# Optimization experiments

Hardware: AMD Instinct MI355X
Metric: run time of the kernel (lower is better)

Reference implementation:

```python
import jax, jax.numpy as jnp
import numpy as np

ATT_WIDTH = 512  # attention_width from init

def _band_mask(T, width, dtype):
    # tf.matrix_band_part(ones, width//2, (width-1)//2): keep i-j<=lower and j-i<=upper
    lower = width // 2
    upper = (width - 1) // 2
    i = jnp.arange(T)[:, None]
    j = jnp.arange(T)[None, :]
    keep = (i - j <= lower) & (j - i <= upper)
    return keep.astype(dtype)

def setup_inputs() -> dict:
    key = jax.random.key(0)
    k1, k2, k3, k4 = jax.random.split(key, 4)
    B, T, H, D = 8, 2048, 1024, 1024
    scale = 1.0 / np.sqrt(H)  # keep activations sane
    return {
        "inputs": jax.random.normal(k1, (B, T, H), dtype=jnp.float32),
        "WQ": jax.random.normal(k2, (H, D), dtype=jnp.float32) * scale,
        "WK": jax.random.normal(k3, (H, D), dtype=jnp.float32) * scale,
        "WV": jax.random.normal(k4, (H, D), dtype=jnp.float32) * scale,
    }

def reference(inputs, WQ, WK, WV) -> jnp.ndarray:
    B, T, H = inputs.shape
    D = WQ.shape[1]
    scale = jnp.asarray(D, inputs.dtype) ** 0.5
    q = jnp.einsum('bth,hd->btd', inputs, WQ)
    k = jnp.einsum('bth,hd->btd', inputs, WK)
    v = jnp.einsum('bth,hd->btd', inputs, WV)
    score = jnp.einsum('bqd,bkd->bqk', q, k) / scale  # [B,T,T]
    # NOTE: original multiplies score by the 0/1 band mask BEFORE softmax
    # (masked entries become 0, not -inf). Faithful reproduction.
    local = _band_mask(T, ATT_WIDTH, score.dtype)
    score = score * local[None, :, :]
    attn = jax.nn.softmax(score, axis=-1)
    return jnp.einsum('bqk,bkd->bqd', attn, v)
```

## Files before the change

### kernel.cpp

```cpp
#include <hip/hip_runtime.h>
#include <hip/hip_bf16.h>
#include <stdint.h>

typedef __attribute__((ext_vector_type(8))) short bf16x8;
typedef __attribute__((ext_vector_type(4))) short short4v;
typedef __attribute__((ext_vector_type(4))) float f32x4;

#define DEV static __device__ __forceinline__

DEV float bf2f(short u) {
    union { float f; uint32_t i; } c; c.i = ((uint32_t)(uint16_t)u) << 16; return c.f;
}
DEV short f2bf(float f) {
    union { float f; uint32_t i; } c; c.f = f;
    uint32_t i = c.i;
    uint32_t r = i + 0x7FFFu + ((i >> 16) & 1u);
    return (short)(r >> 16);
}

DEV void gload_lds16(const short* g, short* l) {
    __builtin_amdgcn_global_load_lds(
        (const __attribute__((address_space(1))) void*)g,
        (__attribute__((address_space(3))) void*)l,
        16, 0, 0);
}

__global__ __launch_bounds__(256)
void cvt_f32_bf16(const float* __restrict__ in, short* __restrict__ out) {
    long i = ((long)blockIdx.x * 256 + threadIdx.x) * 8;
    float4 a = *(const float4*)&in[i];
    float4 b = *(const float4*)&in[i + 4];
    bf16x8 o;
    o[0] = f2bf(a.x); o[1] = f2bf(a.y); o[2] = f2bf(a.z); o[3] = f2bf(a.w);
    o[4] = f2bf(b.x); o[5] = f2bf(b.y); o[6] = f2bf(b.z); o[7] = f2bf(b.w);
    *(bf16x8*)&out[i] = o;
}

__global__ __launch_bounds__(256)
void cvt2_f32_bf16(const float* __restrict__ inA, short* __restrict__ outA,
                   const float* __restrict__ inB, short* __restrict__ outB) {
    int blk = blockIdx.x;
    const float* in = (blk < 512) ? inA : inB;
    short* out      = (blk < 512) ? outA : outB;
    long i = ((long)(blk & 511) * 256 + threadIdx.x) * 8;
    float4 a = *(const float4*)&in[i];
    float4 b = *(const float4*)&in[i + 4];
    bf16x8 o;
    o[0] = f2bf(a.x); o[1] = f2bf(a.y); o[2] = f2bf(a.z); o[3] = f2bf(a.w);
    o[4] = f2bf(b.x); o[5] = f2bf(b.y); o[6] = f2bf(b.z); o[7] = f2bf(b.w);
    *(bf16x8*)&out[i] = o;
}

__global__ __launch_bounds__(256)
void transpose_w(const float* __restrict__ W, short* __restrict__ Wt) {
    const int HD = 1024;
    __shared__ float tile[32][33];
    int bx = blockIdx.x, by = blockIdx.y;
    int tx = threadIdx.x & 31, ty = threadIdx.x >> 5;
    #pragma unroll
    for (int r = ty; r < 32; r += 8)
        tile[r][tx] = W[(long)(by * 32 + r) * HD + bx * 32 + tx];
    __syncthreads();
    #pragma unroll
    for (int r = ty; r < 32; r += 8)
        Wt[(long)(bx * 32 + r) * HD + by * 32 + tx] = f2bf(tile[tx][r]);
}

__global__ __launch_bounds__(256)
void reduce_mt(const float* __restrict__ Mpart, short* __restrict__ MTb) {
    const long SL = 1024L * 1024;
    long i = ((long)blockIdx.x * 256 + threadIdx.x) * 8;
    float s[8];
    #pragma unroll
    for (int j = 0; j < 8; ++j) s[j] = 0.f;
    #pragma unroll
    for (int sl = 0; sl < 4; ++sl) {
        float4 a = *(const float4*)&Mpart[sl * SL + i];
        float4 b = *(const float4*)&Mpart[sl * SL + i + 4];
        s[0] += a.x; s[1] += a.y; s[2] += a.z; s[3] += a.w;
        s[4] += b.x; s[5] += b.y; s[6] += b.z; s[7] += b.w;
    }
    bf16x8 o;
    #pragma unroll
    for (int j = 0; j < 8; ++j) o[j] = f2bf(s[j]);
    *(bf16x8*)&MTb[i] = o;
}


DEV void stage_half(const short* __restrict__ src, int ld, short* dst, int tid) {
    int rr = tid >> 3;
    int cs = ((tid & 7) ^ (rr & 7)) << 3;
    short* d = dst + ((tid >> 6) << 9);
    gload_lds16(src + (long)rr * ld + cs, d);
    gload_lds16(src + (long)(rr + 64) * ld + cs, d + 4096);
}

DEV bf16x8 ld_frag(const short* half, int rowbase, int ks, int lane) {
    int row = rowbase + (lane & 15);
    int idx = (row << 6) + ks * 32 + ((lane >> 4) << 3);
    idx ^= (lane & 7) << 3;
    return *(const bf16x8*)&half[idx];
}

#define SCHED0 __builtin_amdgcn_sched_barrier(0)
#define SBAR do { SCHED0; __builtin_amdgcn_s_barrier(); SCHED0; } while (0)
#define VM(n)  do { asm volatile("s_waitcnt vmcnt(" #n ")" ::: "memory"); SCHED0; } while (0)
#define PRIO1 __builtin_amdgcn_s_setprio(1)
#define PRIO0 __builtin_amdgcn_s_setprio(0)

#define READ_A(HP, QM)                                                          \
    do { _Pragma("unroll") for (int iq = 0; iq < 4; ++iq)                       \
         _Pragma("unroll") for (int ks = 0; ks < 2; ++ks)                       \
             ra[iq][ks] = ld_frag(HP, (QM)*64 + iq*16, ks, lane); } while (0)

#define READ_B(HP, QN)                                                          \
    do { _Pragma("unroll") for (int jn = 0; jn < 2; ++jn)                       \
         _Pragma("unroll") for (int ks = 0; ks < 2; ++ks)                       \
             rb[QN][jn][ks] = ld_frag(HP, wn1*64 + (QN)*32 + jn*16, ks, lane); } while (0)

#define MFMA_Q(QM, QN)                                                          \
    do { _Pragma("unroll") for (int iq = 0; iq < 4; ++iq)                       \
         _Pragma("unroll") for (int jn = 0; jn < 2; ++jn)                       \
         _Pragma("unroll") for (int ks = 0; ks < 2; ++ks)                       \
             acc[(QM)*4+iq][(QN)*2+jn] = __builtin_amdgcn_mfma_f32_16x16x32_bf16( \
                 ra[iq][ks], rb[QN][jn][ks], acc[(QM)*4+iq][(QN)*2+jn], 0,0,0); } while (0)

template<int EPI>
__global__ __launch_bounds__(512, 2)
void gemm256(const short* __restrict__ Abase, const short* __restrict__ Bbase,
             void* __restrict__ o0, void* __restrict__ o1, void* __restrict__ o2,
             const float* __restrict__ Crow, const float* __restrict__ Vsum)
{
    const int T = 2048, HD = 1024;
    __shared__ __align__(16) short lds[2][2][2][8192];

    const int tid  = threadIdx.x;
    const int lane = tid & 63;
    const int w    = tid >> 6;
    const int wm   = w >> 2;
    const int wn   = w & 3;
    const int wn1  = wn & 1;

    int m0, n0, klo, khi, ldA, ldB, bz;
    const short *A, *B;
    if (EPI == 0) {
        int p = (int)blockIdx.x + 8 * (int)blockIdx.y;
        int lid = (p & 7) * 64 + (p >> 3);
        m0 = (lid >> 3) * 256; n0 = (lid & 7) * 256;
        klo = 0; khi = 1024; ldA = HD; ldB = HD; bz = 0;
        A = Abase; B = Bbase;
    } else if (EPI == 1) {
        int p = (int)blockIdx.x + 3 * ((int)blockIdx.y + 8 * (int)blockIdx.z);
        bz = p & 7; int rem = p >> 3;
        int mb = rem / 3, kb = mb + rem % 3 - 1;
        if (kb < 0 || kb > 7) return;
        m0 = mb * 256; n0 = kb * 256;
        klo = 0; khi = 1024; ldA = HD; ldB = HD;
        A = Abase + (long)bz * T * HD; B = Bbase + (long)bz * T * HD;
    } else if (EPI == 2) {
        int p = (int)blockIdx.x + 4 * ((int)blockIdx.y + 8 * (int)blockIdx.z);
        bz = p & 7; int rem = p >> 3;
        int mb = rem / 4;
        m0 = mb * 256; n0 = (rem % 4) * 256;
        klo = max(m0 - 256, 0); khi = min(m0 + 512, T);
        ldA = T; ldB = T;
        A = Abase + (long)bz * T * T; B = Bbase + (long)bz * HD * T;
    } else {
        m0 = blockIdx.y * 256; n0 = blockIdx.x * 256;
        klo = (int)blockIdx.z * 256; khi = klo + 256;
        ldA = HD; ldB = HD; bz = 0;
        A = Abase; B = Bbase;
    }

    const short* Asrc = A + (long)m0 * ldA + klo;
    const short* Bsrc = B + (long)n0 * ldB + klo;
    const short* hA0 = &lds[0][0][wm][0];
    const short* hA1 = &lds[1][0][wm][0];
    const short* hB0 = &lds[0][1][wn >> 1][0];
    const short* hB1 = &lds[1][1][wn >> 1][0];

    auto stA = [&](int bf, int hf, int t) {
        stage_half(Asrc + (long)hf * 128 * ldA + t * 64, ldA, (short*)&lds[bf][0][hf][0], tid); };
    auto stB = [&](int bf, int hf, int t) {
        stage_half(Bsrc + (long)hf * 128 * ldB + t * 64, ldB, (short*)&lds[bf][1][hf][0], tid); };

    f32x4 acc[8][4];
    #pragma unroll
    for (int i = 0; i < 8; ++i)
        #pragma unroll
        for (int j = 0; j < 4; ++j) { acc[i][j][0]=0.f; acc[i][j][1]=0.f; acc[i][j][2]=0.f; acc[i][j][3]=0.f; }
    bf16x8 ra[4][2];
    bf16x8 rb[2][2][2];

    const int NT = (khi - klo) >> 6;

    stB(0,0,0); stB(0,1,0); stA(0,0,0); stA(0,1,0); stB(1,0,1); stB(1,1,1);
    SCHED0; VM(4); SBAR;
    READ_B(hB0, 0); SCHED0;

    #pragma unroll 1
    for (int i = 0; i < NT/2 - 1; ++i) {
        int t1 = 2*i+1, t2 = 2*i+2, t3 = 2*i+3;
        SBAR; READ_A(hA0,0); SCHED0; READ_B(hB0,1); SCHED0; stA(1,0,t1); SCHED0;
        PRIO1; MFMA_Q(0,0); PRIO0; SCHED0;
        SBAR; stA(1,1,t1); SCHED0; PRIO1; MFMA_Q(0,1); PRIO0; SCHED0;
        SBAR; READ_A(hA0,1); SCHED0; stB(0,0,t2); SCHED0;
        PRIO1; MFMA_Q(1,0); PRIO0; SCHED0; VM(2); SCHED0;
        SBAR; READ_B(hB1,0); SCHED0; stB(0,1,t2); SCHED0;
        PRIO1; MFMA_Q(1,1); PRIO0; SCHED0;
        SBAR; READ_A(hA1,0); SCHED0; READ_B(hB1,1); SCHED0; stA(0,0,t2); SCHED0;
        PRIO1; MFMA_Q(0,0); PRIO0; SCHED0;
        SBAR; stA(0,1,t2); SCHED0; PRIO1; MFMA_Q(0,1); PRIO0; SCHED0;
        SBAR; READ_A(hA1,1); SCHED0; stB(1,0,t3); SCHED0;
        PRIO1; MFMA_Q(1,0); PRIO0; SCHED0; VM(2); SCHED0;
        SBAR; READ_B(hB0,0); SCHED0; stB(1,1,t3); SCHED0;
        PRIO1; MFMA_Q(1,1); PRIO0; SCHED0;
    }
    {
        int t1 = NT - 1;
        SBAR; READ_A(hA0,0); SCHED0; READ_B(hB0,1); SCHED0; stA(1,0,t1); SCHED0;
        PRIO1; MFMA_Q(0,0); PRIO0; SCHED0;
        SBAR; stA(1,1,t1); SCHED0; PRIO1; MFMA_Q(0,1); PRIO0; SCHED0;
        SBAR; READ_A(hA0,1); SCHED0;
        PRIO1; MFMA_Q(1,0); PRIO0; SCHED0; VM(0); SCHED0;
        SBAR; READ_B(hB1,0); SCHED0; PRIO1; MFMA_Q(1,1); PRIO0; SCHED0;
        SBAR; READ_A(hA1,0); SCHED0; READ_B(hB1,1); SCHED0;
        PRIO1; MFMA_Q(0,0); PRIO0; SCHED0;
        SBAR; PRIO1; MFMA_Q(0,1); PRIO0; SCHED0;
        SBAR; READ_A(hA1,1); SCHED0; PRIO1; MFMA_Q(1,0); PRIO0; SCHED0;
        SBAR; PRIO1; MFMA_Q(1,1); PRIO0; SCHED0;
    }

    const int fr = lane & 15, fq = lane >> 4;
    const int rbase = m0 + wm * 128, cbase = n0 + wn * 64;

    if (EPI == 0) {
        const int wsel = n0 >> 10;
        if (wsel == 0) {
            short* dst = (short*)o0;
            #pragma unroll
            for (int mi = 0; mi < 8; ++mi)
                #pragma unroll
                for (int ni = 0; ni < 4; ++ni)
                    #pragma unroll
                    for (int r = 0; r < 4; ++r) {
                        int row = rbase + mi * 16 + fq * 4 + r;
                        int col = cbase + ni * 16 + fr;
                        dst[(long)row * HD + col] = f2bf(acc[mi][ni][r]);
                    }
        } else {
            short* Vt = (short*)o2;
            #pragma unroll
            for (int mi = 0; mi < 8; ++mi)
                #pragma unroll
                for (int ni = 0; ni < 4; ++ni) {
                    int col  = (cbase + ni * 16 + fr) & 1023;
                    int row0 = rbase + mi * 16 + fq * 4;
                    int b = row0 >> 11, t = row0 & 2047;
                    short4v v;
                    #pragma unroll
                    for (int r = 0; r < 4; ++r) v[r] = f2bf(acc[mi][ni][r]);
                    *(short4v*)&Vt[((long)b * HD + col) * T + t] = v;
                }
        }
    } else if (EPI == 1) {
        short* S = (short*)o0 + (long)bz * T * T;
        #pragma unroll
        for (int mi = 0; mi < 8; ++mi)
            #pragma unroll
            for (int ni = 0; ni < 4; ++ni)
                #pragma unroll
                for (int r = 0; r < 4; ++r) {
                    int i = rbase + mi * 16 + fq * 4 + r;
                    int j = cbase + ni * 16 + fr;
                    bool keep = (i - j <= 256) && (j - i <= 255);
                    S[(long)i * T + j] = f2bf(keep ? acc[mi][ni][r] * (1.f/32.f) : 0.f);
                }
    } else if (EPI == 2) {
        float* out = (float*)o0;
        #pragma unroll
        for (int mi = 0; mi < 8; ++mi)
            #pragma unroll
            for (int r = 0; r < 4; ++r) {
                int i = rbase + mi * 16 + fq * 4 + r;
                float ci = Crow[bz * T + i];
                #pragma unroll
                for (int ni = 0; ni < 4; ++ni) {
                    int col = cbase + ni * 16 + fr;
                    out[((long)bz * T + i) * HD + col] = acc[mi][ni][r] + ci * Vsum[bz * HD + col];
                }
            }
    } else {
        float* dst = (float*)o0 + (long)blockIdx.z * HD * HD;
        #pragma unroll
        for (int mi = 0; mi < 8; ++mi)
            #pragma unroll
            for (int ni = 0; ni < 4; ++ni)
                #pragma unroll
                for (int r = 0; r < 4; ++r) {
                    int row = rbase + mi * 16 + fq * 4 + r;
                    int col = cbase + ni * 16 + fr;
                    dst[(long)row * HD + col] = acc[mi][ni][r];
                }
    }
}

__global__ __launch_bounds__(256)
void softmax_band(short* __restrict__ S, float* __restrict__ Crow) {
    const int T = 2048;
    int wid = (int)blockIdx.x * 4 + (threadIdx.x >> 6);
    int lane = threadIdx.x & 63;
    int b = wid >> 11, t = wid & 2047;
    int mb = t >> 7;
    int tlo = max(mb - 2, 0) * 128;
    int thi = min(mb + 2, 15) * 128 + 128;
    int nvec = (thi - tlo) >> 3;
    short* row = S + ((long)b * T + t) * T + tlo;

    bool h0 = lane < nvec;
    bool h1 = lane + 64 < nvec;
    bf16x8 v0, v1;
    float f0[8], f1[8];
    float m = 0.f;
    if (h0) {
        v0 = *(const bf16x8*)&row[lane * 8];
        #pragma unroll
        for (int j = 0; j < 8; ++j) { f0[j] = bf2f(v0[j]); m = fmaxf(m, f0[j]); }
    }
    if (h1) {
        v1 = *(const bf16x8*)&row[(lane + 64) * 8];
        #pragma unroll
        for (int j = 0; j < 8; ++j) { f1[j] = bf2f(v1[j]); m = fmaxf(m, f1[j]); }
    }
    #pragma unroll
    for (int o = 32; o; o >>= 1) m = fmaxf(m, __shfl_xor(m, o));

    float e0[8], e1[8];
    float sum = 0.f;
    if (h0) {
        #pragma unroll
        for (int j = 0; j < 8; ++j) { e0[j] = __expf(f0[j] - m); sum += e0[j]; }
    }
    if (h1) {
        #pragma unroll
        for (int j = 0; j < 8; ++j) { e1[j] = __expf(f1[j] - m); sum += e1[j]; }
    }
    #pragma unroll
    for (int o = 32; o; o >>= 1) sum += __shfl_xor(sum, o);
    float em = __expf(-m);
    sum += (float)(2048 - nvec * 8) * em;
    float inv = 1.f / sum;
    float c = em * inv;

    if (h0) {
        #pragma unroll
        for (int j = 0; j < 8; ++j) v0[j] = f2bf(e0[j] * inv - c);
        *(bf16x8*)&row[lane * 8] = v0;
    }
    if (h1) {
        #pragma unroll
        for (int j = 0; j < 8; ++j) v1[j] = f2bf(e1[j] * inv - c);
        *(bf16x8*)&row[(lane + 64) * 8] = v1;
    }
    if (lane == 0) Crow[wid] = c;
}

__global__ __launch_bounds__(256)
void vsum_rows(const short* __restrict__ Vt, float* __restrict__ Vsum) {
    int rowid = (int)blockIdx.x * 4 + (threadIdx.x >> 6);
    int lane = threadIdx.x & 63;
    const short* r = Vt + (long)rowid * 2048;
    float s = 0.f;
    #pragma unroll
    for (int v = 0; v < 4; ++v) {
        bf16x8 x = *(const bf16x8*)&r[(lane + v * 64) * 8];
        #pragma unroll
        for (int j = 0; j < 8; ++j) s += bf2f(x[j]);
    }
    #pragma unroll
    for (int o = 32; o; o >>= 1) s += __shfl_xor(s, o);
    if (lane == 0) Vsum[rowid] = s;
}

extern "C" void kernel_launch(void* const* d_in, const int* in_sizes, int n_in,
                              void* d_out, int out_size, void* d_ws, size_t ws_size,
                              hipStream_t stream) {
    const int B = 8, T = 2048, H = 1024, D = 1024;
    const long MT = (long)B * T;

    const float* X  = (const float*)d_in[0];
    const float* WQ = (const float*)d_in[1];
    const float* WK = (const float*)d_in[2];
    const float* WV = (const float*)d_in[3];
    float* out = (float*)d_out;

    char* ws = (char*)d_ws;
    size_t off = 0;
    auto alloc = [&](size_t bytes) {
        char* p = ws + off;
        off += (bytes + 255) & ~(size_t)255;
        return p;
    };
    short* Xb    = (short*)alloc(MT * H * 2);
    short* WQb   = (short*)alloc((long)H * D * 2);
    short* WKb   = (short*)alloc((long)H * D * 2);
    short* Bfuse = (short*)alloc(2L * D * H * 2);
    short* MTb   = Bfuse;
    short* WVt   = Bfuse + (long)D * H;
    float* Mpart = (float*)alloc(4L * D * H * 4);
    short* Gb    = (short*)alloc(MT * D * 2);
    short* Vt    = (short*)alloc((long)B * D * T * 2);
    short* S     = (short*)alloc((long)B * T * T * 2);
    float* Crow  = (float*)alloc(MT * 4);
    float* Vsum  = (float*)alloc((long)B * D * 4);
    if (off > ws_size) return;

    cvt_f32_bf16<<<(int)(MT * H / 2048), 256, 0, stream>>>(X, Xb);
    cvt2_f32_bf16<<<1024, 256, 0, stream>>>(WQ, WQb, WK, WKb);
    transpose_w<<<dim3(32, 32), 256, 0, stream>>>(WV, WVt);

    gemm256<3><<<dim3(4, 4, 4), 512, 0, stream>>>(WKb, WQb, Mpart, nullptr, nullptr, nullptr, nullptr);
    reduce_mt<<<512, 256, 0, stream>>>(Mpart, MTb);

    gemm256<0><<<dim3(8, 64, 1), 512, 0, stream>>>(Xb, Bfuse, Gb, nullptr, Vt, nullptr, nullptr);

    vsum_rows<<<(int)(B * D / 4), 256, 0, stream>>>(Vt, Vsum);

    gemm256<1><<<dim3(3, 8, B), 512, 0, stream>>>(Gb, Xb, S, nullptr, nullptr, nullptr, nullptr);

    softmax_band<<<(int)(MT / 4), 256, 0, stream>>>(S, Crow);

    gemm256<2><<<dim3(4, 8, B), 512, 0, stream>>>(S, Vt, out, nullptr, nullptr, Crow, Vsum);
}
```

Measured before the change: 212.0 us.

## Restructure GEMM main loop into uniform phases with explicit barriers and waits

Rewrites the software-pipelined GEMM main loop as eight uniform phases. Each phase issues one LDS fragment read plus one global-to-LDS stage, then barriers, waits on lgkmcnt(0), and runs one MFMA quadrant followed by a second barrier. The fragment reads and the vmcnt waits are redistributed across phases so loads overlap the MFMAs more evenly. This adds a second barrier per phase and explicit LDS waits, which may serialize the waves more and cut overlap.

```diff
diff --git a/kernel.cpp b/kernel.cpp
--- a/kernel.cpp
+++ b/kernel.cpp
@@ -104,6 +104,7 @@
 
 #define SCHED0 __builtin_amdgcn_sched_barrier(0)
 #define SBAR do { SCHED0; __builtin_amdgcn_s_barrier(); SCHED0; } while (0)
+#define LGK0 do { asm volatile("s_waitcnt lgkmcnt(0)" ::: "memory"); SCHED0; } while (0)
 #define VM(n)  do { asm volatile("s_waitcnt vmcnt(" #n ")" ::: "memory"); SCHED0; } while (0)
 #define PRIO1 __builtin_amdgcn_s_setprio(1)
 #define PRIO0 __builtin_amdgcn_s_setprio(0)
@@ -124,6 +125,9 @@
          _Pragma("unroll") for (int ks = 0; ks < 2; ++ks)                       \
              acc[(QM)*4+iq][(QN)*2+jn] = __builtin_amdgcn_mfma_f32_16x16x32_bf16( \
                  ra[iq][ks], rb[QN][jn][ks], acc[(QM)*4+iq][(QN)*2+jn], 0,0,0); } while (0)
+
+#define PHASE(PRE, Q1, Q2)                                                      \
+    do { PRE; SBAR; LGK0; PRIO1; MFMA_Q(Q1, Q2); PRIO0; SBAR; } while (0)
 
 template<int EPI>
 __global__ __launch_bounds__(512, 2)
@@ -201,34 +205,25 @@
     #pragma unroll 1
     for (int i = 0; i < NT/2 - 1; ++i) {
         int t1 = 2*i+1, t2 = 2*i+2, t3 = 2*i+3;
-        SBAR; READ_A(hA0,0); SCHED0; READ_B(hB0,1); SCHED0; stA(1,0,t1); SCHED0;
-        PRIO1; MFMA_Q(0,0); PRIO0; SCHED0;
-        SBAR; stA(1,1,t1); SCHED0; PRIO1; MFMA_Q(0,1); PRIO0; SCHED0;
-        SBAR; READ_A(hA0,1); SCHED0; stB(0,0,t2); SCHED0;
-        PRIO1; MFMA_Q(1,0); PRIO0; SCHED0; VM(2); SCHED0;
-        SBAR; READ_B(hB1,0); SCHED0; stB(0,1,t2); SCHED0;
-        PRIO1; MFMA_Q(1,1); PRIO0; SCHED0;
-        SBAR; READ_A(hA1,0); SCHED0; READ_B(hB1,1); SCHED0; stA(0,0,t2); SCHED0;
-        PRIO1; MFMA_Q(0,0); PRIO0; SCHED0;
-        SBAR; stA(0,1,t2); SCHED0; PRIO1; MFMA_Q(0,1); PRIO0; SCHED0;
-        SBAR; READ_A(hA1,1); SCHED0; stB(1,0,t3); SCHED0;
-        PRIO1; MFMA_Q(1,0); PRIO0; SCHED0; VM(2); SCHED0;
-        SBAR; READ_B(hB0,0); SCHED0; stB(1,1,t3); SCHED0;
-        PRIO1; MFMA_Q(1,1); PRIO0; SCHED0;
+        PHASE( READ_A(hA0,0); SCHED0; stA(1,0,t1); SCHED0          , 0, 0);
+        PHASE( READ_B(hB0,1); SCHED0; stA(1,1,t1); SCHED0          , 0, 1);
+        PHASE( READ_A(hA0,1); SCHED0; stB(0,0,t2); SCHED0; VM(6)   , 1, 0);
+        PHASE( READ_B(hB1,0); SCHED0; stB(0,1,t2); SCHED0; VM(4)   , 1, 1);
+        PHASE( READ_A(hA1,0); SCHED0; stA(0,0,t2); SCHED0          , 0, 0);
+        PHASE( READ_B(hB1,1); SCHED0; stA(0,1,t2); SCHED0          , 0, 1);
+        PHASE( READ_A(hA1,1); SCHED0; stB(1,0,t3); SCHED0; VM(6)   , 1, 0);
+        PHASE( READ_B(hB0,0); SCHED0; stB(1,1,t3); SCHED0; VM(4)   , 1, 1);
     }
     {
         int t1 = NT - 1;
-        SBAR; READ_A(hA0,0); SCHED0; READ_B(hB0,1); SCHED0; stA(1,0,t1); SCHED0;
-        PRIO1; MFMA_Q(0,0); PRIO0; SCHED0;
-        SBAR; stA(1,1,t1); SCHED0; PRIO1; MFMA_Q(0,1); PRIO0; SCHED0;
-        SBAR; READ_A(hA0,1); SCHED0;
-        PRIO1; MFMA_Q(1,0); PRIO0; SCHED0; VM(0); SCHED0;
-        SBAR; READ_B(hB1,0); SCHED0; PRIO1; MFMA_Q(1,1); PRIO0; SCHED0;
-        SBAR; READ_A(hA1,0); SCHED0; READ_B(hB1,1); SCHED0;
-        PRIO1; MFMA_Q(0,0); PRIO0; SCHED0;
-        SBAR; PRIO1; MFMA_Q(0,1); PRIO0; SCHED0;
-        SBAR; READ_A(hA1,1); SCHED0; PRIO1; MFMA_Q(1,0); PRIO0; SCHED0;
-        SBAR; PRIO1; MFMA_Q(1,1); PRIO0; SCHED0;
+        PHASE( READ_A(hA0,0); SCHED0; stA(1,0,t1); SCHED0          , 0, 0);
+        PHASE( READ_B(hB0,1); SCHED0; stA(1,1,t1); SCHED0          , 0, 1);
+        PHASE( READ_A(hA0,1); SCHED0; VM(4)                        , 1, 0);
+        PHASE( READ_B(hB1,0); SCHED0; VM(0)                        , 1, 1);
+        PHASE( READ_A(hA1,0); SCHED0                               , 0, 0);
+        PHASE( READ_B(hB1,1); SCHED0                               , 0, 1);
+        PHASE( READ_A(hA1,1); SCHED0                               , 1, 0);
+        SBAR; LGK0; PRIO1; MFMA_Q(1,1); PRIO0; SCHED0;
     }
 
     const int fr = lane & 15, fq = lane >> 4;
```

After: 217.3 us. 2.5% more time.
